# Kernel tuning notes

Hardware: AMD Instinct MI355X
Metric: run time of the kernel (lower is better)

Reference implementation:

```python
import jax, jax.numpy as jnp
import numpy as np

K = 3          # deformable kernel size
N = K * K      # sampling points per output pixel
PAD = 1
BN_EPS = 1e-5


def setup_inputs() -> dict:
    key = jax.random.key(0)
    ks = jax.random.split(key, 6)
    B, C, H, W = 32, 103, 32, 32
    Cout = 32
    x = jax.random.normal(ks[0], (B, C, H, W), jnp.float32)
    # offset-predicting conv: 2*N output channels (N y-offsets then N x-offsets)
    w_off = jax.random.normal(ks[1], (2 * N, C, K, K), jnp.float32) * 0.01
    b_off = jnp.zeros((2 * N,), jnp.float32)
    # main deformable conv weight
    w = jax.random.normal(ks[2], (Cout, C, K, K), jnp.float32) * (1.0 / np.sqrt(C * N))
    b = jnp.zeros((Cout,), jnp.float32)
    # BatchNorm (eval mode) params
    gamma = jax.random.uniform(ks[3], (Cout,), jnp.float32, 0.5, 1.5)
    beta = jax.random.normal(ks[4], (Cout,), jnp.float32) * 0.1
    run_mean = jax.random.normal(ks[5], (Cout,), jnp.float32) * 0.1
    run_var = jnp.ones((Cout,), jnp.float32)
    return {"x": x, "w_off": w_off, "b_off": b_off, "w": w, "b": b,
            "gamma": gamma, "beta": beta, "run_mean": run_mean, "run_var": run_var}


def _deform_conv(x, w_off, b_off, w, b):
    B, C, H, W = x.shape
    # predicted offsets: (B, 2N, H, W) -> (B, H, W, N) each for y and x
    off = jax.lax.conv_general_dilated(x, w_off, (1, 1), [(PAD, PAD), (PAD, PAD)])
    off = off + b_off[None, :, None, None]
    off_y = jnp.transpose(off[:, :N], (0, 2, 3, 1))
    off_x = jnp.transpose(off[:, N:], (0, 2, 3, 1))
    # regular kernel grid offsets p_n in {-1,0,1}^2
    ky, kx = jnp.meshgrid(jnp.arange(-1, 2, dtype=jnp.float32),
                          jnp.arange(-1, 2, dtype=jnp.float32), indexing='ij')
    kn_y, kn_x = ky.reshape(-1), kx.reshape(-1)  # (N,)
    # base grid p_0 in padded coordinates (stride 1, padding 1 -> starts at 1)
    p0_y = jnp.arange(1, H + 1, dtype=jnp.float32)[None, :, None, None]
    p0_x = jnp.arange(1, W + 1, dtype=jnp.float32)[None, None, :, None]
    Hp, Wp = H + 2 * PAD, W + 2 * PAD
    py = jnp.clip(p0_y + kn_y + off_y, 0.0, Hp - 1.0)  # (B,H,W,N)
    px = jnp.clip(p0_x + kn_x + off_x, 0.0, Wp - 1.0)
    # zero-padded input, flattened spatial for gather
    xp = jnp.pad(x, ((0, 0), (0, 0), (PAD, PAD), (PAD, PAD)))
    xf = xp.reshape(B, C, Hp * Wp)
    y0 = jnp.clip(jnp.floor(py).astype(jnp.int32), 0, Hp - 2)
    x0 = jnp.clip(jnp.floor(px).astype(jnp.int32), 0, Wp - 2)
    y1, x1 = y0 + 1, x0 + 1
    wy = (py - y0.astype(py.dtype))[:, None]  # (B,1,H,W,N)
    wx = (px - x0.astype(px.dtype))[:, None]

    def gather(yi, xi):
        idx = (yi * Wp + xi).reshape(B, -1)                      # (B, H*W*N)
        g = jnp.take_along_axis(xf, idx[:, None, :], axis=2)    # (B, C, H*W*N)
        return g.reshape(B, C, H, W, N)

    v00, v01 = gather(y0, x0), gather(y0, x1)
    v10, v11 = gather(y1, x0), gather(y1, x1)
    samp = (v00 * (1 - wy) * (1 - wx) + v01 * (1 - wy) * wx
            + v10 * wy * (1 - wx) + v11 * wy * wx)               # (B,C,H,W,N)
    out = jnp.einsum('bchwn,ocn->bohw', samp, w.reshape(w.shape[0], C, N))
    return out + b[None, :, None, None]


def reference(x, w_off, b_off, w, b, gamma, beta, run_mean, run_var):
    out = _deform_conv(x, w_off, b_off, w, b)
    # BatchNorm2d (eval mode) + ReLU
    inv = gamma * jax.lax.rsqrt(run_var + BN_EPS)
    out = out * inv[None, :, None, None] + (beta - run_mean * inv)[None, :, None, None]
    return jax.nn.relu(out)
```

## Files before the change

### kernel.cpp

```cpp
#include <hip/hip_runtime.h>


#define CC    103
#define COUT  32
#define KSC   5
#define RSU   34
#define PLSU  1164
#define NPAIR 8
#define BUF_U (NPAIR * PLSU)

typedef __attribute__((ext_vector_type(8))) _Float16 f16x8;
typedef __attribute__((ext_vector_type(2))) _Float16 h2;
typedef __attribute__((ext_vector_type(2))) __fp16  fp16x2;
typedef __attribute__((ext_vector_type(4))) float f32x4;

#define WTPM_W 0
#define WTPO_W 17920
#define BN_W   35840
#define XPK_W  35904

__global__ void k_prep(const float* __restrict__ x,
                       const float* __restrict__ w, const float* __restrict__ w_off,
                       const float* __restrict__ bias, const float* __restrict__ gamma,
                       const float* __restrict__ beta, const float* __restrict__ mean,
                       const float* __restrict__ var,
                       unsigned short* __restrict__ wtpm, unsigned short* __restrict__ wtpo,
                       float* __restrict__ bn, unsigned int* __restrict__ xpk) {
    int bx = blockIdx.x;
    if (bx < 280) {
        int tid = bx * 256 + threadIdx.x;
        if (tid < 71680) {
            int half_ = tid >= 35840 ? 1 : 0;
            int e = tid - half_ * 35840;
            const float* src = half_ ? w_off : w;
            unsigned short* dst = half_ ? wtpo : wtpm;
            int mrows = half_ ? 18 : 32;
            int j = e & 7, lane = (e >> 3) & 63, tile = e >> 9;
            int mt = tile & 1, chs = tile >> 1;
            int s = chs % 5, ch = chs / 5;
            int o = mt * 16 + (lane & 15);
            int kl = s * 32 + (lane >> 4) * 8 + j;
            int n = kl >> 4, c = ch * 16 + (kl & 15);
            float v = 0.f;
            if (n < 9 && c < CC && o < mrows) v = src[o * (CC * 9) + c * 9 + n];
            union { _Float16 h; unsigned short u; } cv;
            cv.h = (_Float16)v;
            dst[e] = cv.u;
        }
        if (tid < 32) {
            float inv = gamma[tid] * rsqrtf(var[tid] + 1e-5f);
            bn[tid]      = inv;
            bn[32 + tid] = beta[tid] + (bias[tid] - mean[tid]) * inv;
        }
    } else {
        int pb = bx - 280;
        int b = pb / 7, ch = pb - b * 7;
        int tl = threadIdx.x;
        const float* xb = x + b * (CC * 1024) + tl * 4;
        unsigned int* dst = xpk + pb * 8192 + tl * 4;
#pragma unroll
        for (int i = 0; i < NPAIR; i++) {
            int c = ch * 16 + 2 * i;
            float4 L = make_float4(0.f, 0.f, 0.f, 0.f);
            float4 M = make_float4(0.f, 0.f, 0.f, 0.f);
            if (c < CC)     L = *(const float4*)(xb + c * 1024);
            if (c + 1 < CC) M = *(const float4*)(xb + (c + 1) * 1024);
            union { fp16x2 hh; unsigned u; } p0, p1, p2, p3;
            p0.hh = __builtin_amdgcn_cvt_pkrtz(L.x, M.x);
            p1.hh = __builtin_amdgcn_cvt_pkrtz(L.y, M.y);
            p2.hh = __builtin_amdgcn_cvt_pkrtz(L.z, M.z);
            p3.hh = __builtin_amdgcn_cvt_pkrtz(L.w, M.w);
            *(uint4*)(dst + i * 1024) = make_uint4(p0.u, p1.u, p2.u, p3.u);
        }
    }
}

__global__ void __launch_bounds__(512, 4)
k_fused(const unsigned int* __restrict__ xpk, const float* __restrict__ b_off,
        const unsigned short* __restrict__ wtpo, const unsigned short* __restrict__ wtpm,
        const float* __restrict__ bn, float* __restrict__ out) {
    __shared__ unsigned int ldsp[2 * BUF_U];
    __shared__ float exch[18 * 64];

    int bid = blockIdx.x;
    int b   = (bid & 7) * 4 + ((bid >> 3) & 3);
    int pxg = bid >> 5;

    int t = threadIdx.x, lane = t & 63, wv = t >> 6;
    int kh = wv >> 2;
    int pxl = (wv & 3) * 16 + (lane & 15);
    int px  = pxg * 64 + pxl;
    int h = px >> 5, wq = px & 31;
    int kg = lane >> 4;
    int hi = kg >> 1;
    int pb = (kg & 1) * 4;

    unsigned int* mybuf = ldsp + kh * BUF_U;

    int tl = t & 255;
    int sr = tl >> 3, sk = (tl & 7) * 4;

    int r0 = 2 * pxg - 1; if (r0 < 0) r0 = 0;
    int r1 = 2 * pxg + 2; if (r1 > 31) r1 = 31;
    bool rowact = (sr >= r0 && sr <= r1);

    const int KYL[5] = {0,0,1,2,2}, KXL[5] = {0,2,1,0,2};
    const int KYH[5] = {0,1,1,2,2}, KXH[5] = {1,0,2,1,2};
    const int TAPL[5] = {0,2,4,6,8}, TAPH[5] = {1,3,5,7,8};
    int myky[5], mykx[5], mytap[5];
#pragma unroll
    for (int s = 0; s < 5; s++) {
        myky[s] = hi ? KYH[s] : KYL[s];
        mykx[s] = hi ? KXH[s] : KXL[s];
        mytap[s] = hi ? TAPH[s] : TAPL[s];
    }

    uint4 U[NPAIR];
    auto loadx = [&](int ch, bool full) {
        if (!full && !rowact) return;
        const unsigned int* s0 = xpk + (b * 7 + ch) * 8192 + tl * 4;
#pragma unroll
        for (int i = 0; i < NPAIR; i++) U[i] = *(const uint4*)(s0 + i * 1024);
    };
    auto packwrite = [&](int ch, bool full) {
        if (!full && !rowact) return;
        unsigned int* dstb = mybuf + (sr + 1) * RSU + 2 + sk;
#pragma unroll
        for (int i = 0; i < NPAIR; i++) {
            *(uint2*)(dstb + i * PLSU)     = make_uint2(U[i].x, U[i].y);
            *(uint2*)(dstb + i * PLSU + 2) = make_uint2(U[i].z, U[i].w);
        }
    };

    auto chunk1 = [&](int it) { return kh ? (2 * it) : (it < 3 ? 2 * it + 1 : -1); };
    auto chunk2 = [&](int it) { return kh ? (6 - 2 * it) : (it < 3 ? 5 - 2 * it : -1); };
    int fullIt = 2 + kh;

    f32x4 acc0 = {0.f, 0.f, 0.f, 0.f};
    f32x4 acc1 = {0.f, 0.f, 0.f, 0.f};

    loadx(chunk1(0), false);
    for (int i = t; i < 2240; i += 512) {
        int plane = i / 140, r = i - plane * 140;
        int off;
        if (r < 34)      off = r;
        else if (r < 76) off = 1122 + (r - 34);
        else { int rr = (r - 76) >> 1; off = (rr + 1) * 34 + ((r - 76) & 1); }
        ldsp[(plane >> 3) * BUF_U + (plane & 7) * PLSU + off] = 0u;
    }
    __syncthreads();

    for (int it = 0; it < 4; it++) {
        int ch = chunk1(it);
        if (ch >= 0) packwrite(ch, it == fullIt);
        __syncthreads();
        int nx = (it < 3) ? chunk1(it + 1) : -1;
        if (nx >= 0) loadx(nx, it + 1 == fullIt);
        if (ch >= 0) {
            const unsigned short* wch = wtpo + ch * 5120;
#pragma unroll
            for (int s = 0; s < KSC; s++) {
                const unsigned int* cell = mybuf + pb * PLSU
                    + (h + myky[s]) * RSU + 1 + (wq + mykx[s]);
                union { unsigned u[4]; f16x8 v; } bu;
#pragma unroll
                for (int jj = 0; jj < 4; jj++) bu.u[jj] = cell[jj * PLSU];
                f16x8 a0 = *(const f16x8*)(wch + s * 1024 + lane * 8);
                f16x8 a1 = *(const f16x8*)(wch + s * 1024 + 512 + lane * 8);
                acc0 = __builtin_amdgcn_mfma_f32_16x16x32_f16(a0, bu.v, acc0, 0, 0, 0);
                acc1 = __builtin_amdgcn_mfma_f32_16x16x32_f16(a1, bu.v, acc1, 0, 0, 0);
            }
        }
        __syncthreads();
    }

    if (kh == 0) {
        float* ex = exch + pxl;
#pragma unroll
        for (int reg = 0; reg < 4; reg++) ex[(kg * 4 + reg) * 64] = acc0[reg];
        if (kg == 0) { ex[16 * 64] = acc1[0]; ex[17 * 64] = acc1[1]; }
    }
    __syncthreads();
    if (kh == 1) {
        float* ex = exch + pxl;
#pragma unroll
        for (int reg = 0; reg < 4; reg++) ex[(kg * 4 + reg) * 64] += acc0[reg];
        if (kg == 0) { ex[16 * 64] += acc1[0]; ex[17 * 64] += acc1[1]; }
    }
    __syncthreads();

    int cofs[KSC];
    h2  W[KSC][4];
#pragma unroll
    for (int s = 0; s < KSC; s++) {
        int tap = mytap[s];
        float oy = exch[tap * 64 + pxl] + b_off[tap];
        float ox = exch[(9 + tap) * 64 + pxl] + b_off[9 + tap];
        float py  = (float)(h + myky[s]) + oy;
        float pxx = (float)(wq + mykx[s]) + ox;
        py  = fminf(fmaxf(py, 0.f), 33.f);
        pxx = fminf(fmaxf(pxx, 0.f), 33.f);
        int y0 = min((int)py, 32);
        int x0 = min((int)pxx, 32);
        float fy = py - (float)y0;
        float fx = pxx - (float)x0;
        float w00 = (1.f - fy) * (1.f - fx), w01 = (1.f - fy) * fx;
        float w10 = fy * (1.f - fx),          w11 = fy * fx;
        W[s][0] = (h2){(_Float16)w00, (_Float16)w00};
        W[s][1] = (h2){(_Float16)w01, (_Float16)w01};
        W[s][2] = (h2){(_Float16)w10, (_Float16)w10};
        W[s][3] = (h2){(_Float16)w11, (_Float16)w11};
        cofs[s] = pb * PLSU + y0 * RSU + 1 + x0;
    }

    acc0 = (f32x4){0.f, 0.f, 0.f, 0.f};
    acc1 = (f32x4){0.f, 0.f, 0.f, 0.f};
    for (int it = 0; it < 4; it++) {
        int ch = chunk2(it);
        if (it > 0) {
            if (ch >= 0) packwrite(ch, true);
            else {
                float* e = (float*)ldsp + pxl;
#pragma unroll
                for (int reg = 0; reg < 4; reg++) {
                    e[(kg * 4 + reg) * 64]      = acc0[reg];
                    e[(16 + kg * 4 + reg) * 64] = acc1[reg];
                }
            }
        }
        __syncthreads();
        int nx = (it < 3) ? chunk2(it + 1) : -1;
        if (nx >= 0) loadx(nx, true);
        if (ch >= 0) {
            const unsigned short* wch = wtpm + ch * 5120;
#pragma unroll
            for (int s = 0; s < KSC; s++) {
                const unsigned int* cell = mybuf + cofs[s];
                union { unsigned u[4]; f16x8 v; } bu;
#pragma unroll
                for (int jj = 0; jj < 4; jj++) {
                    union { unsigned u; h2 hh; } t0, t1, b0, b1;
                    t0.u = cell[jj * PLSU];
                    t1.u = cell[jj * PLSU + 1];
                    b0.u = cell[jj * PLSU + RSU];
                    b1.u = cell[jj * PLSU + RSU + 1];
                    h2 sm = t0.hh * W[s][0] + t1.hh * W[s][1]
                          + b0.hh * W[s][2] + b1.hh * W[s][3];
                    union { h2 hh; unsigned u; } r; r.hh = sm;
                    bu.u[jj] = r.u;
                }
                f16x8 a0 = *(const f16x8*)(wch + s * 1024 + lane * 8);
                f16x8 a1 = *(const f16x8*)(wch + s * 1024 + 512 + lane * 8);
                acc0 = __builtin_amdgcn_mfma_f32_16x16x32_f16(a0, bu.v, acc0, 0, 0, 0);
                acc1 = __builtin_amdgcn_mfma_f32_16x16x32_f16(a1, bu.v, acc1, 0, 0, 0);
            }
        }
        __syncthreads();
    }

    if (kh == 1) {
        const float* ex2 = (const float*)ldsp;
        float* op = out + (size_t)b * COUT * 1024 + px;
#pragma unroll
        for (int mt = 0; mt < 2; mt++) {
            f32x4 a = mt ? acc1 : acc0;
#pragma unroll
            for (int reg = 0; reg < 4; reg++) {
                int o = mt * 16 + kg * 4 + reg;
                float tot = a[reg] + ex2[o * 64 + pxl];
                float v = tot * bn[o] + bn[32 + o];
                op[o * 1024] = fmaxf(v, 0.f);
            }
        }
    }
}

extern "C" void kernel_launch(void* const* d_in, const int* in_sizes, int n_in,
                              void* d_out, int out_size, void* d_ws, size_t ws_size,
                              hipStream_t stream) {
    const float* x      = (const float*)d_in[0];
    const float* w_off  = (const float*)d_in[1];
    const float* b_off  = (const float*)d_in[2];
    const float* w      = (const float*)d_in[3];
    const float* bias   = (const float*)d_in[4];
    const float* gamma  = (const float*)d_in[5];
    const float* beta   = (const float*)d_in[6];
    const float* rmean  = (const float*)d_in[7];
    const float* rvar   = (const float*)d_in[8];
    float* out = (float*)d_out;

    float* ws = (float*)d_ws;
    unsigned short* wtpm = (unsigned short*)(ws + WTPM_W);
    unsigned short* wtpo = (unsigned short*)(ws + WTPO_W);
    float*          bn   = ws + BN_W;
    unsigned int*   xpk  = (unsigned int*)(ws + XPK_W);

    k_prep <<<504, 256, 0, stream>>>(x, w, w_off, bias, gamma, beta, rmean, rvar,
                                     wtpm, wtpo, bn, xpk);
    k_fused<<<512, 512, 0, stream>>>(xpk, b_off, wtpo, wtpm, bn, out);
}
```

Measured before the change: 103.8 us.

## Interleave channel pairs per pixel in LDS for 128-bit sample reads

Changes the packed fp16 x layout in global memory and in LDS. Each pixel now holds four channel-pair words contiguously, grouped into two groups of four pairs, instead of one plane per channel pair. Every B-operand gather, both the regular offset-conv taps and the four bilinear corners, becomes a single 128-bit LDS load instead of four scalar loads. The zero-fill of padding uses vector stores, and global loads and the output stores use nontemporal hints. The interleaved layout may cause more LDS bank conflicts on the unaligned bilinear corner reads.

```diff
diff --git a/kernel.cpp b/kernel.cpp
--- a/kernel.cpp
+++ b/kernel.cpp
@@ -5,14 +5,14 @@
 #define COUT  32
 #define KSC   5
 #define RSU   34
-#define PLSU  1164
-#define NPAIR 8
-#define BUF_U (NPAIR * PLSU)
+#define GS_D  4656
+#define BUF_U (2 * GS_D)
 
 typedef __attribute__((ext_vector_type(8))) _Float16 f16x8;
 typedef __attribute__((ext_vector_type(2))) _Float16 h2;
 typedef __attribute__((ext_vector_type(2))) __fp16  fp16x2;
 typedef __attribute__((ext_vector_type(4))) float f32x4;
+typedef __attribute__((ext_vector_type(4))) unsigned int u32x4;
 
 #define WTPM_W 0
 #define WTPO_W 17920
@@ -57,9 +57,10 @@
         int b = pb / 7, ch = pb - b * 7;
         int tl = threadIdx.x;
         const float* xb = x + b * (CC * 1024) + tl * 4;
-        unsigned int* dst = xpk + pb * 8192 + tl * 4;
-#pragma unroll
-        for (int i = 0; i < NPAIR; i++) {
+        unsigned int* dst = xpk + pb * 8192 + tl * 16;
+        unsigned d[8][4];
+#pragma unroll
+        for (int i = 0; i < 8; i++) {
             int c = ch * 16 + 2 * i;
             float4 L = make_float4(0.f, 0.f, 0.f, 0.f);
             float4 M = make_float4(0.f, 0.f, 0.f, 0.f);
@@ -70,7 +71,12 @@
             p1.hh = __builtin_amdgcn_cvt_pkrtz(L.y, M.y);
             p2.hh = __builtin_amdgcn_cvt_pkrtz(L.z, M.z);
             p3.hh = __builtin_amdgcn_cvt_pkrtz(L.w, M.w);
-            *(uint4*)(dst + i * 1024) = make_uint4(p0.u, p1.u, p2.u, p3.u);
+            d[i][0] = p0.u; d[i][1] = p1.u; d[i][2] = p2.u; d[i][3] = p3.u;
+        }
+#pragma unroll
+        for (int q = 0; q < 4; q++) {
+            *(u32x4*)(dst + q * 4)        = (u32x4){d[0][q], d[1][q], d[2][q], d[3][q]};
+            *(u32x4*)(dst + 4096 + q * 4) = (u32x4){d[4][q], d[5][q], d[6][q], d[7][q]};
         }
     }
 }
@@ -79,7 +85,7 @@
 k_fused(const unsigned int* __restrict__ xpk, const float* __restrict__ b_off,
         const unsigned short* __restrict__ wtpo, const unsigned short* __restrict__ wtpm,
         const float* __restrict__ bn, float* __restrict__ out) {
-    __shared__ unsigned int ldsp[2 * BUF_U];
+    __shared__ __align__(16) unsigned int ldsp[2 * BUF_U];
     __shared__ float exch[18 * 64];
 
     int bid = blockIdx.x;
@@ -93,16 +99,16 @@
     int h = px >> 5, wq = px & 31;
     int kg = lane >> 4;
     int hi = kg >> 1;
-    int pb = (kg & 1) * 4;
+    int kgrp = kg & 1;
 
     unsigned int* mybuf = ldsp + kh * BUF_U;
 
     int tl = t & 255;
-    int sr = tl >> 3, sk = (tl & 7) * 4;
+    int r = tl >> 3, c = tl & 7;
 
     int r0 = 2 * pxg - 1; if (r0 < 0) r0 = 0;
     int r1 = 2 * pxg + 2; if (r1 > 31) r1 = 31;
-    bool rowact = (sr >= r0 && sr <= r1);
+    bool rowact = (r >= r0 && r <= r1);
 
     const int KYL[5] = {0,0,1,2,2}, KXL[5] = {0,2,1,0,2};
     const int KYH[5] = {0,1,1,2,2}, KXH[5] = {1,0,2,1,2};
@@ -115,21 +121,25 @@
         mytap[s] = hi ? TAPH[s] : TAPL[s];
     }
 
-    uint4 U[NPAIR];
+    u32x4 U[8];
     auto loadx = [&](int ch, bool full) {
         if (!full && !rowact) return;
-        const unsigned int* s0 = xpk + (b * 7 + ch) * 8192 + tl * 4;
-#pragma unroll
-        for (int i = 0; i < NPAIR; i++) U[i] = *(const uint4*)(s0 + i * 1024);
+        const unsigned int* s0 = xpk + (b * 7 + ch) * 8192 + (r * 32 + c) * 4;
+#pragma unroll
+        for (int g = 0; g < 2; g++)
+#pragma unroll
+        for (int k = 0; k < 4; k++)
+            U[g * 4 + k] = __builtin_nontemporal_load(
+                               (const u32x4*)(s0 + g * 4096 + k * 32));
     };
     auto packwrite = [&](int ch, bool full) {
         if (!full && !rowact) return;
-        unsigned int* dstb = mybuf + (sr + 1) * RSU + 2 + sk;
-#pragma unroll
-        for (int i = 0; i < NPAIR; i++) {
-            *(uint2*)(dstb + i * PLSU)     = make_uint2(U[i].x, U[i].y);
-            *(uint2*)(dstb + i * PLSU + 2) = make_uint2(U[i].z, U[i].w);
-        }
+        unsigned int* dstb = mybuf + ((r + 1) * RSU + 2 + c) * 4;
+#pragma unroll
+        for (int g = 0; g < 2; g++)
+#pragma unroll
+        for (int k = 0; k < 4; k++)
+            *(u32x4*)(dstb + g * GS_D + k * 32) = U[g * 4 + k];
     };
 
     auto chunk1 = [&](int it) { return kh ? (2 * it) : (it < 3 ? 2 * it + 1 : -1); };
@@ -140,13 +150,16 @@
     f32x4 acc1 = {0.f, 0.f, 0.f, 0.f};
 
     loadx(chunk1(0), false);
-    for (int i = t; i < 2240; i += 512) {
-        int plane = i / 140, r = i - plane * 140;
-        int off;
-        if (r < 34)      off = r;
-        else if (r < 76) off = 1122 + (r - 34);
-        else { int rr = (r - 76) >> 1; off = (rr + 1) * 34 + ((r - 76) & 1); }
-        ldsp[(plane >> 3) * BUF_U + (plane & 7) * PLSU + off] = 0u;
+    {
+        u32x4 z4 = (u32x4){0u, 0u, 0u, 0u};
+        for (int i = t; i < 560; i += 512) {
+            int grp = i / 140, rr = i - grp * 140;
+            int off;
+            if (rr < 34)      off = rr;
+            else if (rr < 76) off = 1122 + (rr - 34);
+            else { int q2 = (rr - 76) >> 1; off = (q2 + 1) * 34 + ((rr - 76) & 1); }
+            *(u32x4*)(ldsp + (grp >> 1) * BUF_U + (grp & 1) * GS_D + off * 4) = z4;
+        }
     }
     __syncthreads();
 
@@ -160,11 +173,10 @@
             const unsigned short* wch = wtpo + ch * 5120;
 #pragma unroll
             for (int s = 0; s < KSC; s++) {
-                const unsigned int* cell = mybuf + pb * PLSU
-                    + (h + myky[s]) * RSU + 1 + (wq + mykx[s]);
-                union { unsigned u[4]; f16x8 v; } bu;
-#pragma unroll
-                for (int jj = 0; jj < 4; jj++) bu.u[jj] = cell[jj * PLSU];
+                const unsigned int* cell = mybuf + kgrp * GS_D
+                    + ((h + myky[s]) * RSU + 1 + (wq + mykx[s])) * 4;
+                union { u32x4 q; f16x8 v; } bu;
+                bu.q = *(const u32x4*)cell;
                 f16x8 a0 = *(const f16x8*)(wch + s * 1024 + lane * 8);
                 f16x8 a1 = *(const f16x8*)(wch + s * 1024 + 512 + lane * 8);
                 acc0 = __builtin_amdgcn_mfma_f32_16x16x32_f16(a0, bu.v, acc0, 0, 0, 0);
@@ -210,7 +222,7 @@
         W[s][1] = (h2){(_Float16)w01, (_Float16)w01};
         W[s][2] = (h2){(_Float16)w10, (_Float16)w10};
         W[s][3] = (h2){(_Float16)w11, (_Float16)w11};
-        cofs[s] = pb * PLSU + y0 * RSU + 1 + x0;
+        cofs[s] = kgrp * GS_D + (y0 * RSU + 1 + x0) * 4;
     }
 
     acc0 = (f32x4){0.f, 0.f, 0.f, 0.f};
@@ -236,18 +248,22 @@
 #pragma unroll
             for (int s = 0; s < KSC; s++) {
                 const unsigned int* cell = mybuf + cofs[s];
+                union { u32x4 q; unsigned a[4]; } T0, T1, B0, B1;
+                T0.q = *(const u32x4*)(cell);
+                T1.q = *(const u32x4*)(cell + 4);
+                B0.q = *(const u32x4*)(cell + 4 * RSU);
+                B1.q = *(const u32x4*)(cell + 4 * RSU + 4);
                 union { unsigned u[4]; f16x8 v; } bu;
 #pragma unroll
                 for (int jj = 0; jj < 4; jj++) {
-                    union { unsigned u; h2 hh; } t0, t1, b0, b1;
-                    t0.u = cell[jj * PLSU];
-                    t1.u = cell[jj * PLSU + 1];
-                    b0.u = cell[jj * PLSU + RSU];
-                    b1.u = cell[jj * PLSU + RSU + 1];
-                    h2 sm = t0.hh * W[s][0] + t1.hh * W[s][1]
+                    union { unsigned u; h2 hh; } t0, t1, b0, b1, rr;
+                    t0.u = T0.a[jj];
+                    t1.u = T1.a[jj];
+                    b0.u = B0.a[jj];
+                    b1.u = B1.a[jj];
+                    rr.hh = t0.hh * W[s][0] + t1.hh * W[s][1]
                           + b0.hh * W[s][2] + b1.hh * W[s][3];
-                    union { h2 hh; unsigned u; } r; r.hh = sm;
-                    bu.u[jj] = r.u;
+                    bu.u[jj] = rr.u;
                 }
                 f16x8 a0 = *(const f16x8*)(wch + s * 1024 + lane * 8);
                 f16x8 a1 = *(const f16x8*)(wch + s * 1024 + 512 + lane * 8);
@@ -269,7 +285,7 @@
                 int o = mt * 16 + kg * 4 + reg;
                 float tot = a[reg] + ex2[o * 64 + pxl];
                 float v = tot * bn[o] + bn[32 + o];
-                op[o * 1024] = fmaxf(v, 0.f);
+                __builtin_nontemporal_store(fmaxf(v, 0.f), &op[o * 1024]);
             }
         }
     }
```

After: 102.0 us. No clear change (-1.7%).
